# Kernel tuning notes

Measured on AMD Instinct MI355X. Metric: run time of the kernel, lower is better.

Reference implementation:

```python
import jax, jax.numpy as jnp
import numpy as np

DIM = 512
HID = 1024        # dim * expansion_factor
QK = 128          # query_key_dim
G = 256           # group_size
EPS = 1e-5


def setup_inputs() -> dict:
    key = jax.random.key(0)
    ks = jax.random.split(key, 6)
    x = jax.random.normal(ks[0], (4, 4096, DIM), jnp.float32)
    ln_w = jnp.ones((DIM,), jnp.float32)
    ln_b = jnp.zeros((DIM,), jnp.float32)
    Wh = 0.02 * jax.random.normal(ks[1], (DIM, 2 * HID), jnp.float32)
    bh = jnp.zeros((2 * HID,), jnp.float32)
    Wqk = 0.02 * jax.random.normal(ks[2], (DIM, QK), jnp.float32)
    bqk = jnp.zeros((QK,), jnp.float32)
    gamma = 0.02 * jax.random.normal(ks[3], (4, QK), jnp.float32)  # nn.init.normal_(gamma, std=0.02)
    beta = jnp.zeros((4, QK), jnp.float32)
    Wo = 0.02 * jax.random.normal(ks[4], (HID, DIM), jnp.float32)
    bo = jnp.zeros((DIM,), jnp.float32)
    return {"x": x, "ln_w": ln_w, "ln_b": ln_b, "Wh": Wh, "bh": bh,
            "Wqk": Wqk, "bqk": bqk, "gamma": gamma, "beta": beta,
            "Wo": Wo, "bo": bo}


def reference(x, ln_w, ln_b, Wh, bh, Wqk, bqk, gamma, beta, Wo, bo):
    b, n, _ = x.shape
    g = n // G  # number of groups (n chosen as multiple of G -> no padding)

    # LayerNorm (torch uses biased variance)
    mu = jnp.mean(x, axis=-1, keepdims=True)
    var = jnp.mean((x - mu) ** 2, axis=-1, keepdims=True)
    normed = (x - mu) * jax.lax.rsqrt(var + EPS) * ln_w + ln_b

    # to_hidden: Linear -> SiLU, split into v / gate
    h = jax.nn.silu(normed @ Wh + bh)            # [b, n, 2*HID]
    v, gate = jnp.split(h, 2, axis=-1)           # each [b, n, HID]

    # to_qk: Linear -> SiLU, then 4-head offset/scale
    qk = jax.nn.silu(normed @ Wqk + bqk)         # [b, n, QK]
    qkh = qk[..., None, :] * gamma + beta        # [b, n, 4, QK]
    quad_q, lin_q, quad_k, lin_k = (qkh[..., i, :] for i in range(4))

    # group: b (g n) d -> b g n d
    grp = lambda t: t.reshape(b, g, G, t.shape[-1])
    qq, qk_, lq, lk, vv = map(grp, (quad_q, quad_k, lin_q, lin_k, v))

    # quadratic (group-local) attention with ReLU^2 scores, causal within group
    sim = jnp.einsum('bgid,bgjd->bgij', qq, qk_) / G
    attn = jnp.square(jnp.maximum(sim, 0.0))
    causal_mask = jnp.triu(jnp.ones((G, G), dtype=bool), 1)
    attn = jnp.where(causal_mask, 0.0, attn)
    quad_out = jnp.einsum('bgij,bgje->bgie', attn, vv)   # [b, g, G, HID]

    # linear attention across groups: per-group kv, exclusive cumsum over group dim
    lin_kv = jnp.einsum('bgnd,bgne->bgde', lk, vv) / G   # [b, g, QK, HID]
    lin_kv = jnp.cumsum(lin_kv, axis=1)
    lin_kv = jnp.pad(lin_kv, ((0, 0), (1, 0), (0, 0), (0, 0)))[:, :-1]
    lin_out = jnp.einsum('bgde,bgnd->bgne', lin_kv, lq)  # [b, g, G, HID]

    out = gate * (quad_out.reshape(b, n, HID) + lin_out.reshape(b, n, HID))
    return out @ Wo + bo + x
```

## Files before the change

kernel.cpp:

```cpp
#include <hip/hip_runtime.h>
#include <hip/hip_bf16.h>
#include <math.h>


#define BATCH 4
#define SEQ   4096
#define TROWS 16384
#define DIMD  512
#define HIDD  1024
#define QKD   128
#define GRP   256
#define NGRP  16
#define BGRP  64
#define EPIW  132

typedef unsigned short bfraw;
typedef __attribute__((ext_vector_type(8))) short bf16x8;
typedef __attribute__((ext_vector_type(8))) unsigned short u16x8;
typedef __attribute__((ext_vector_type(4))) unsigned int u32x4;
typedef __attribute__((ext_vector_type(4))) float f32x4;

__device__ __forceinline__ float bf2f(bfraw u) {
    union { float f; unsigned int i; } c;
    c.i = ((unsigned int)u) << 16;
    return c.f;
}
__device__ __forceinline__ bfraw f2bf(float f) {
    unsigned int x = __float_as_uint(f);
    unsigned int r = (x + 0x7fffu + ((x >> 16) & 1u)) >> 16;
    return (bfraw)r;
}
__device__ __forceinline__ unsigned int pkbf(float lo, float hi) {
    __hip_bfloat162 h2 = __float22bfloat162_rn(make_float2(lo, hi));
    union { __hip_bfloat162 h; unsigned int u; } c; c.h = h2;
    return c.u;
}
__device__ __forceinline__ void store16bf(bfraw* dst, const float* src) {
    u32x4 a, b;
    #pragma unroll
    for (int k = 0; k < 4; ++k) a[k] = pkbf(src[2 * k], src[2 * k + 1]);
    #pragma unroll
    for (int k = 0; k < 4; ++k) b[k] = pkbf(src[8 + 2 * k], src[8 + 2 * k + 1]);
    *(u32x4*)dst = a;
    *(u32x4*)(dst + 8) = b;
}
__device__ __forceinline__ void store8bf(bfraw* dst, const float* src) {
    u32x4 a;
    #pragma unroll
    for (int k = 0; k < 4; ++k) a[k] = pkbf(src[2 * k], src[2 * k + 1]);
    *(u32x4*)dst = a;
}
__device__ __forceinline__ float silu_f(float z) {
    return z / (1.f + __expf(-z));
}
__device__ __forceinline__ void gload_lds16(const void* g, void* l) {
    __builtin_amdgcn_global_load_lds(
        (const __attribute__((address_space(1))) unsigned int*)g,
        (__attribute__((address_space(3))) unsigned int*)l, 16, 0, 0);
}

__device__ __forceinline__ void mfma_step(const bfraw* As, const bfraw* Bs,
                                          f32x4 acc[4][4], int wm, int wn,
                                          int q, int mi) {
    bf16x8 af[4], bfg[4];
    #pragma unroll
    for (int i = 0; i < 4; ++i)
        af[i] = *(const bf16x8*)&As[(size_t)(wm * 64 + i * 16 + mi) * 32 + q * 8];
    #pragma unroll
    for (int j = 0; j < 4; ++j)
        bfg[j] = *(const bf16x8*)&Bs[(size_t)(wn * 64 + j * 16 + mi) * 32 + q * 8];
    #pragma unroll
    for (int i = 0; i < 4; ++i)
        #pragma unroll
        for (int j = 0; j < 4; ++j)
            acc[i][j] = __builtin_amdgcn_mfma_f32_16x16x32_bf16(af[i], bfg[j], acc[i][j], 0, 0, 0);
}

#define SMEMP_DECL                                              \
    __shared__ __align__(16) char smem_[33280];                 \
    bfraw* A0buf = (bfraw*)smem_;                               \
    bfraw* B0buf = (bfraw*)(smem_ + 8192);                      \
    bfraw* A1buf = (bfraw*)(smem_ + 16384);                     \
    bfraw* B1buf = (bfraw*)(smem_ + 24576);

#define PIPE_DSTS                                               \
    bfraw* a0d  = A0buf + wid * 512;                            \
    bfraw* a0d2 = A0buf + 2048 + wid * 512;                     \
    bfraw* b0d  = B0buf + wid * 512;                            \
    bfraw* b0d2 = B0buf + 2048 + wid * 512;                     \
    bfraw* a1d  = A1buf + wid * 512;                            \
    bfraw* a1d2 = A1buf + 2048 + wid * 512;                     \
    bfraw* b1d  = B1buf + wid * 512;                            \
    bfraw* b1d2 = B1buf + 2048 + wid * 512;

#define KLOOP_PRE(Abase, Astr, Bbase, Bstr)                                    \
    const bfraw* pa0 = (Abase) + (size_t)(t >> 2) * (Astr) + (t & 3) * 8;      \
    const bfraw* pa1 = pa0 + (size_t)64 * (Astr);                              \
    const bfraw* pb0 = (Bbase) + (size_t)(t >> 2) * (Bstr) + (t & 3) * 8;      \
    const bfraw* pb1 = pb0 + (size_t)64 * (Bstr);

#define STAGE0                                                                 \
    do { gload_lds16(pa0, a0d); gload_lds16(pa1, a0d2);                        \
         gload_lds16(pb0, b0d); gload_lds16(pb1, b0d2);                        \
         pa0 += 32; pa1 += 32; pb0 += 32; pb1 += 32; } while (0)
#define STAGE1                                                                 \
    do { gload_lds16(pa0, a1d); gload_lds16(pa1, a1d2);                        \
         gload_lds16(pb0, b1d); gload_lds16(pb1, b1d2);                        \
         pa0 += 32; pa1 += 32; pb0 += 32; pb1 += 32; } while (0)

#define PIPE_LOOP(NIT, Abase, Astr, Bbase, Bstr)                               \
    {                                                                          \
        KLOOP_PRE(Abase, Astr, Bbase, Bstr)                                    \
        STAGE0;                                                                \
        for (int it = 0; it < (NIT); it += 2) {                                \
            __syncthreads();                                                   \
            if (it + 1 < (NIT)) STAGE1;                                        \
            mfma_step(A0buf, B0buf, acc, wm, wn, q, mi);                       \
            __syncthreads();                                                   \
            if (it + 2 < (NIT)) STAGE0;                                        \
            if (it + 1 < (NIT))                                                \
                mfma_step(A1buf, B1buf, acc, wm, wn, q, mi);                   \
        }                                                                      \
        __syncthreads();                                                       \
    }

__device__ __forceinline__ int epi_row(int p, int lr) {
    return (lr < 16) ? (p * 16 + lr) : (64 + p * 16 + (lr - 16));
}

__global__ __launch_bounds__(256) void prep_kernel(const float* __restrict__ x,
                                                   const float* __restrict__ lnw,
                                                   const float* __restrict__ lnb,
                                                   const float* __restrict__ Wh,
                                                   const float* __restrict__ Wo,
                                                   const float* __restrict__ Wqk,
                                                   bfraw* __restrict__ normb,
                                                   bfraw* __restrict__ WhT,
                                                   bfraw* __restrict__ WoT,
                                                   bfraw* __restrict__ WqkT) {
    __shared__ float tile[32][33];
    int bid = blockIdx.x;
    int t = threadIdx.x;
    if (bid < 4096) {
        int row  = bid * 4 + (t >> 6);
        int lane = t & 63;
        const float* xr = x + (size_t)row * DIMD;
        float4 v0 = ((const float4*)xr)[lane];
        float4 v1 = ((const float4*)xr)[lane + 64];
        float s  = v0.x + v0.y + v0.z + v0.w + v1.x + v1.y + v1.z + v1.w;
        float ss = v0.x*v0.x + v0.y*v0.y + v0.z*v0.z + v0.w*v0.w
                 + v1.x*v1.x + v1.y*v1.y + v1.z*v1.z + v1.w*v1.w;
        #pragma unroll
        for (int off = 32; off; off >>= 1) {
            s  += __shfl_xor(s, off);
            ss += __shfl_xor(ss, off);
        }
        float mu  = s * (1.f / DIMD);
        float var = ss * (1.f / DIMD) - mu * mu;
        float inv = rsqrtf(var + 1e-5f);
        float4 w0 = ((const float4*)lnw)[lane],  w1 = ((const float4*)lnw)[lane + 64];
        float4 b0 = ((const float4*)lnb)[lane],  b1 = ((const float4*)lnb)[lane + 64];
        unsigned int o0 = pkbf((v0.x - mu) * inv * w0.x + b0.x,
                               (v0.y - mu) * inv * w0.y + b0.y);
        unsigned int o1 = pkbf((v0.z - mu) * inv * w0.z + b0.z,
                               (v0.w - mu) * inv * w0.w + b0.w);
        unsigned int o2 = pkbf((v1.x - mu) * inv * w1.x + b1.x,
                               (v1.y - mu) * inv * w1.y + b1.y);
        unsigned int o3 = pkbf((v1.z - mu) * inv * w1.z + b1.z,
                               (v1.w - mu) * inv * w1.w + b1.w);
        unsigned int* brow = (unsigned int*)(normb + (size_t)row * DIMD);
        ((uint2*)brow)[lane]      = make_uint2(o0, o1);
        ((uint2*)brow)[lane + 64] = make_uint2(o2, o3);
        return;
    }
    bid -= 4096;
    const float* in; bfraw* outp; int R, C, nx;
    if (bid < 1024)      { in = Wh;  outp = WhT;  R = DIMD; C = 2 * HIDD; nx = 64; }
    else if (bid < 1536) { bid -= 1024; in = Wo;  outp = WoT;  R = HIDD; C = DIMD; nx = 16; }
    else                 { bid -= 1536; in = Wqk; outp = WqkT; R = DIMD; C = QKD;  nx = 4; }
    int c0 = (bid % nx) * 32, r0 = (bid / nx) * 32;
    int tr = t >> 3, tc4 = (t & 7) * 4;
    float4 v = *(const float4*)&in[(size_t)(r0 + tr) * C + c0 + tc4];
    tile[tr][tc4 + 0] = v.x; tile[tr][tc4 + 1] = v.y;
    tile[tr][tc4 + 2] = v.z; tile[tr][tc4 + 3] = v.w;
    __syncthreads();
    ushort4 s;
    s.x = f2bf(tile[tc4 + 0][tr]);
    s.y = f2bf(tile[tc4 + 1][tr]);
    s.z = f2bf(tile[tc4 + 2][tr]);
    s.w = f2bf(tile[tc4 + 3][tr]);
    *(ushort4*)&outp[(size_t)(c0 + tr) * R + r0 + tc4] = s;
}

__global__ __launch_bounds__(512, 4) void gemm_h256(
    const bfraw* __restrict__ A,
    const bfraw* __restrict__ WhT,
    const bfraw* __restrict__ WqkT,
    const float* __restrict__ bh,
    const float* __restrict__ bqk,
    const float* __restrict__ gamma,
    const float* __restrict__ beta,
    bfraw* __restrict__ vT,
    bfraw* __restrict__ gate,
    bfraw* __restrict__ qq,
    bfraw* __restrict__ lq,
    bfraw* __restrict__ kk,
    bfraw* __restrict__ lkT) {
    __shared__ __align__(16) char smem_[73728];
    const int t = threadIdx.x;
    const int lane = t & 63, wid = t >> 6;
    const int wm = wid >> 2, wn = wid & 3;
    const int q = lane >> 4, mi = lane & 15;
    int nid = (blockIdx.x & 7) * 144 + (blockIdx.x >> 3);
    const int ct = nid % 9, by = nid / 9;
    const int r0 = by * 128, c0 = ct * 256;
    const int bg = r0 >> 8;
    const int jb0 = r0 & 255;

    const int lslot = (t & 7) ^ ((t >> 3) & 7);
    const int srow  = 2 * (t >> 3) + (lslot >> 2);
    const int skel  = (lslot & 3) * 8;
    const bfraw* Asrc = A + (size_t)(r0 + srow) * DIMD + skel;
    const bfraw* Bsrc0;
    const bfraw* Bsrc1;
    if (ct < 8) {
        Bsrc0 = WhT + (size_t)(c0 + srow) * DIMD + skel;
        Bsrc1 = Bsrc0 + (size_t)128 * DIMD;
    } else {
        Bsrc0 = WqkT + (size_t)srow * DIMD + skel;
        Bsrc1 = Bsrc0;
    }
    const int swz = ((((mi & 1) << 2) | q) ^ ((mi >> 1) & 7)) << 4;
    const int a_off = (wm * 32 + (mi >> 1)) * 128 + swz;
    const int b_off = (wn * 32 + (mi >> 1)) * 128 + swz;

#define GH_STAGE(KT, SLOT)                                                    \
    do {                                                                      \
        char* sb_ = smem_ + (SLOT) * 24576;                                   \
        gload_lds16(Asrc  + (KT) * 32, sb_ + t * 16);                         \
        gload_lds16(Bsrc0 + (KT) * 32, sb_ + 8192 + t * 16);                  \
        gload_lds16(Bsrc1 + (KT) * 32, sb_ + 16384 + t * 16);                 \
    } while (0)

    f32x4 acc[4][4] = {};
    GH_STAGE(0, 0);
    GH_STAGE(1, 1);
    asm volatile("s_waitcnt vmcnt(3)" ::: "memory");
    __builtin_amdgcn_s_barrier();

    #pragma unroll
    for (int j = 0; j < 16; ++j) {
        if (j + 2 < 16) GH_STAGE(j + 2, (j + 2) % 3);
        const char* cb = smem_ + (j % 3) * 24576;
        bf16x8 af[4], bfr[4];
        #pragma unroll
        for (int mf = 0; mf < 4; ++mf)
            af[mf] = *(const bf16x8*)(cb + a_off + mf * 1024);
        #pragma unroll
        for (int nf = 0; nf < 4; ++nf)
            bfr[nf] = *(const bf16x8*)(cb + 8192 + b_off + nf * 1024);
        __builtin_amdgcn_s_setprio(1);
        #pragma unroll
        for (int mf = 0; mf < 4; ++mf)
            #pragma unroll
            for (int nf = 0; nf < 4; ++nf)
                acc[mf][nf] = __builtin_amdgcn_mfma_f32_16x16x32_bf16(
                    af[mf], bfr[nf], acc[mf][nf], 0, 0, 0);
        __builtin_amdgcn_s_setprio(0);
        if (j + 2 < 16)      asm volatile("s_waitcnt vmcnt(3)" ::: "memory");
        else if (j + 1 < 16) asm volatile("s_waitcnt vmcnt(0)" ::: "memory");
        __builtin_amdgcn_s_barrier();
    }
#undef GH_STAGE

    float* epi = (float*)smem_;
    if (ct == 8) {
        float* gbl = (float*)(smem_ + 36864);
        gbl[t] = gamma[t];
        gbl[t + 512] = beta[t];
        float bq4[4];
        #pragma unroll
        for (int nf = 0; nf < 4; ++nf)
            bq4[nf] = (wn < 2) ? bqk[wn * 64 + nf * 16 + mi] : 0.f;
        #pragma unroll
        for (int p2 = 0; p2 < 4; ++p2) {
            if (wm == (p2 >> 1) && wn < 2) {
                #pragma unroll
                for (int mf2 = 0; mf2 < 2; ++mf2) {
                    int mf = ((p2 & 1) << 1) + mf2;
                    #pragma unroll
                    for (int nf = 0; nf < 4; ++nf)
                        #pragma unroll
                        for (int rg = 0; rg < 4; ++rg)
                            epi[(mf2 * 16 + q * 4 + rg) * 132 + wn * 64 + nf * 16 + mi] =
                                silu_f(acc[mf][nf][rg] + bq4[nf]);
                }
            }
            __syncthreads();
            {
                int lr = t >> 4, cs = (t & 15) * 8;
                float z[8];
                #pragma unroll
                for (int k = 0; k < 8; ++k) z[k] = epi[lr * 132 + cs + k];
                size_t growr = (size_t)(r0 + p2 * 32 + lr) * QKD + cs;
                #pragma unroll
                for (int hd = 0; hd < 3; ++hd) {
                    bfraw* arr = (hd == 0) ? qq : (hd == 1) ? lq : kk;
                    float tmp[8];
                    #pragma unroll
                    for (int k = 0; k < 8; ++k)
                        tmp[k] = z[k] * gbl[hd * 128 + cs + k] + gbl[512 + hd * 128 + cs + k];
                    store8bf(arr + growr, tmp);
                }
            }
            {
                int c = t >> 2, jh = (t & 3) * 8;
                float g3 = gbl[384 + c], e3 = gbl[896 + c];
                float tmp[8];
                #pragma unroll
                for (int k = 0; k < 8; ++k)
                    tmp[k] = epi[(jh + k) * 132 + c] * g3 + e3;
                store8bf(lkT + ((size_t)bg * QKD + c) * GRP + jb0 + p2 * 32 + jh, tmp);
            }
            __syncthreads();
        }
        return;
    }
    float bias4[4];
    #pragma unroll
    for (int nf = 0; nf < 4; ++nf)
        bias4[nf] = bh[c0 + wn * 64 + nf * 16 + mi];
    if (ct < 4) {
        #pragma unroll
        for (int p2 = 0; p2 < 4; ++p2) {
            if (wm == (p2 >> 1)) {
                #pragma unroll
                for (int mf2 = 0; mf2 < 2; ++mf2) {
                    int mf = ((p2 & 1) << 1) + mf2;
                    #pragma unroll
                    for (int nf = 0; nf < 4; ++nf)
                        #pragma unroll
                        for (int rg = 0; rg < 4; ++rg)
                            epi[(mf2 * 16 + q * 4 + rg) * 257 + wn * 64 + nf * 16 + mi] =
                                silu_f(acc[mf][nf][rg] + bias4[nf]);
                }
            }
            __syncthreads();
            int e2 = t >> 1, js = (t & 1) * 16;
            float tmp[16];
            #pragma unroll
            for (int k = 0; k < 16; ++k)
                tmp[k] = epi[(js + k) * 257 + e2];
            store16bf(vT + ((size_t)bg * HIDD + c0 + e2) * GRP + jb0 + p2 * 32 + js, tmp);
            __syncthreads();
        }
    } else {
        #pragma unroll
        for (int p2 = 0; p2 < 4; ++p2) {
            if (wm == (p2 >> 1)) {
                #pragma unroll
                for (int mf2 = 0; mf2 < 2; ++mf2) {
                    int mf = ((p2 & 1) << 1) + mf2;
                    #pragma unroll
                    for (int nf = 0; nf < 4; ++nf)
                        #pragma unroll
                        for (int rg = 0; rg < 4; ++rg)
                            epi[(mf2 * 16 + q * 4 + rg) * 260 + wn * 64 + nf * 16 + mi] =
                                silu_f(acc[mf][nf][rg] + bias4[nf]);
                }
            }
            __syncthreads();
            int lr = t >> 4, cs = (t & 15) * 16;
            float tmp[16];
            #pragma unroll
            for (int k = 0; k < 16; ++k)
                tmp[k] = epi[lr * 260 + cs + k];
            store16bf(gate + (size_t)(r0 + p2 * 32 + lr) * HIDD + (c0 - HIDD) + cs, tmp);
            __syncthreads();
        }
    }
}

__global__ __launch_bounds__(256) void simkv_kernel(const bfraw* __restrict__ qq,
                                                    const bfraw* __restrict__ kk,
                                                    bfraw* __restrict__ attn,
                                                    const bfraw* __restrict__ vT,
                                                    const bfraw* __restrict__ lkT,
                                                    bfraw* __restrict__ kvT_raw) {
    SMEMP_DECL
    float* epi = (float*)smem_;
    int t = threadIdx.x;
    int lane = t & 63, wid = t >> 6;
    int wm = wid >> 1, wn = wid & 1;
    int q = lane >> 4, mi = lane & 15;
    int bid = blockIdx.x;
    f32x4 acc[4][4] = {};
    PIPE_DSTS
    if (bid < 512) {
        int bg = bid >> 3;
        int row0 = (bid & 7) * 128;
        PIPE_LOOP(8, vT + (size_t)bg * HIDD * GRP + (size_t)row0 * GRP, GRP,
                  lkT + (size_t)bg * QKD * GRP, GRP)
        bfraw* outg = kvT_raw + (size_t)bg * HIDD * QKD;
        #pragma unroll
        for (int p = 0; p < 4; ++p) {
            #pragma unroll
            for (int j = 0; j < 4; ++j)
                #pragma unroll
                for (int rg = 0; rg < 4; ++rg)
                    epi[(wm * 16 + q * 4 + rg) * EPIW + wn * 64 + j * 16 + mi] = acc[p][j][rg];
            __syncthreads();
            int lr = t >> 3, c0t = (t & 7) * 16;
            int gr = row0 + epi_row(p, lr);
            store16bf(outg + (size_t)gr * QKD + c0t, &epi[lr * EPIW + c0t]);
            __syncthreads();
        }
        return;
    }
    int i = bid - 512;
    int bg = i & 63;
    int tid = i >> 6;
    int ry = (tid == 0) ? 0 : 1;
    int rx = (tid == 2) ? 1 : 0;
    int row0 = ry * 128, col0 = rx * 128;
    PIPE_LOOP(4, qq + (size_t)(bg * GRP + row0) * QKD, QKD,
              kk + (size_t)(bg * GRP + col0) * QKD, QKD)
    bfraw* ag = attn + (size_t)bg * GRP * GRP;
    #pragma unroll
    for (int p = 0; p < 4; ++p) {
        #pragma unroll
        for (int j = 0; j < 4; ++j) {
            int colg = col0 + wn * 64 + j * 16 + mi;
            #pragma unroll
            for (int rg = 0; rg < 4; ++rg) {
                int rowg = row0 + wm * 64 + p * 16 + q * 4 + rg;
                float s = acc[p][j][rg] * (1.f / GRP);
                s = fmaxf(s, 0.f);
                s = s * s;
                epi[(wm * 16 + q * 4 + rg) * EPIW + wn * 64 + j * 16 + mi] =
                    (colg > rowg) ? 0.f : s;
            }
        }
        __syncthreads();
        int lr = t >> 3, c0t = (t & 7) * 16;
        int gr = row0 + epi_row(p, lr);
        store16bf(ag + (size_t)gr * GRP + col0 + c0t, &epi[lr * EPIW + c0t]);
        __syncthreads();
    }
}

__global__ __launch_bounds__(256) void cumsum2_kernel(const bfraw* __restrict__ raw,
                                                      bfraw* __restrict__ ex) {
    int idx = blockIdx.x * 256 + threadIdx.x;
    int b = idx >> 14;
    int r8 = (idx & 16383) * 8;
    const bfraw* rp = raw + (size_t)b * NGRP * 131072 + r8;
    bfraw* ep = ex + (size_t)b * NGRP * 131072 + r8;
    float run[8] = {};
    #pragma unroll
    for (int g = 0; g < NGRP; ++g) {
        u16x8 v = *(const u16x8*)(rp + (size_t)g * 131072);
        store8bf(ep + (size_t)g * 131072, run);
        #pragma unroll
        for (int k = 0; k < 8; ++k)
            run[k] += bf2f(v[k]) * (1.f / GRP);
    }
}

__global__ __launch_bounds__(512, 4) void quadlin256(
    const bfraw* __restrict__ attn,
    const bfraw* __restrict__ vT,
    const bfraw* __restrict__ lq,
    const bfraw* __restrict__ kvT_ex,
    const bfraw* __restrict__ gate,
    bfraw* __restrict__ gated) {
    __shared__ __align__(16) char smem_[73728];
    const int t = threadIdx.x;
    const int lane = t & 63, wid = t >> 6;
    const int wm = wid >> 2, wn = wid & 3;
    const int q = lane >> 4, mi = lane & 15;
    int nid = (blockIdx.x & 7) * 64 + (blockIdx.x >> 3);
    const int bg = nid >> 3;
    const int row0 = ((nid >> 2) & 1) * 128;
    const int c0 = (nid & 3) * 256;

    const int lslot = (t & 7) ^ ((t >> 3) & 7);
    const int srow  = 2 * (t >> 3) + (lslot >> 2);
    const int skel  = (lslot & 3) * 8;
    const bfraw* A1 = attn + ((size_t)bg * GRP + row0 + srow) * GRP + skel;
    const bfraw* B1a = vT + ((size_t)bg * HIDD + c0 + srow) * GRP + skel;
    const bfraw* B1b = B1a + (size_t)128 * GRP;
    const bfraw* A2 = lq + ((size_t)bg * GRP + row0 + srow) * QKD + skel;
    const bfraw* B2a = kvT_ex + ((size_t)bg * HIDD + c0 + srow) * QKD + skel;
    const bfraw* B2b = B2a + (size_t)128 * QKD;

    const int swz = ((((mi & 1) << 2) | q) ^ ((mi >> 1) & 7)) << 4;
    const int a_off = (wm * 32 + (mi >> 1)) * 128 + swz;
    const int b_off = (wn * 32 + (mi >> 1)) * 128 + swz;

#define QL_STAGE(PA, PB0, PB1, KT, SLOT)                                      \
    do {                                                                      \
        char* sb_ = smem_ + (SLOT) * 24576;                                   \
        gload_lds16((PA)  + (KT) * 32, sb_ + t * 16);                         \
        gload_lds16((PB0) + (KT) * 32, sb_ + 8192 + t * 16);                  \
        gload_lds16((PB1) + (KT) * 32, sb_ + 16384 + t * 16);                 \
    } while (0)
#define QL_MFMA(SLOT)                                                         \
    do {                                                                      \
        const char* cb = smem_ + (SLOT) * 24576;                              \
        bf16x8 af[4], bfr[4];                                                 \
        _Pragma("unroll")                                                     \
        for (int mf = 0; mf < 4; ++mf)                                        \
            af[mf] = *(const bf16x8*)(cb + a_off + mf * 1024);                \
        _Pragma("unroll")                                                     \
        for (int nf = 0; nf < 4; ++nf)                                        \
            bfr[nf] = *(const bf16x8*)(cb + 8192 + b_off + nf * 1024);        \
        __builtin_amdgcn_s_setprio(1);                                        \
        _Pragma("unroll")                                                     \
        for (int mf = 0; mf < 4; ++mf)                                        \
            _Pragma("unroll")                                                 \
            for (int nf = 0; nf < 4; ++nf)                                    \
                acc[mf][nf] = __builtin_amdgcn_mfma_f32_16x16x32_bf16(        \
                    af[mf], bfr[nf], acc[mf][nf], 0, 0, 0);                   \
        __builtin_amdgcn_s_setprio(0);                                        \
    } while (0)

    f32x4 acc[4][4] = {};
    const int nit1 = (row0 + 128) >> 5;
    QL_STAGE(A1, B1a, B1b, 0, 0);
    QL_STAGE(A1, B1a, B1b, 1, 1);
    asm volatile("s_waitcnt vmcnt(3)" ::: "memory");
    __builtin_amdgcn_s_barrier();
    for (int j = 0; j < nit1; ++j) {
        if (j + 2 < nit1) QL_STAGE(A1, B1a, B1b, j + 2, (j + 2) % 3);
        QL_MFMA(j % 3);
        if (j + 2 < nit1)      asm volatile("s_waitcnt vmcnt(3)" ::: "memory");
        else if (j + 1 < nit1) asm volatile("s_waitcnt vmcnt(0)" ::: "memory");
        __builtin_amdgcn_s_barrier();
    }
    QL_STAGE(A2, B2a, B2b, 0, 0);
    QL_STAGE(A2, B2a, B2b, 1, 1);
    asm volatile("s_waitcnt vmcnt(3)" ::: "memory");
    __builtin_amdgcn_s_barrier();
    #pragma unroll
    for (int j = 0; j < 4; ++j) {
        if (j + 2 < 4) QL_STAGE(A2, B2a, B2b, j + 2, (j + 2) % 3);
        QL_MFMA(j % 3);
        if (j + 2 < 4)      asm volatile("s_waitcnt vmcnt(3)" ::: "memory");
        else if (j + 1 < 4) asm volatile("s_waitcnt vmcnt(0)" ::: "memory");
        __builtin_amdgcn_s_barrier();
    }
#undef QL_STAGE
#undef QL_MFMA

    float* epi = (float*)smem_;
    #pragma unroll
    for (int p2 = 0; p2 < 4; ++p2) {
        if (wm == (p2 >> 1)) {
            #pragma unroll
            for (int mf2 = 0; mf2 < 2; ++mf2) {
                int mf = ((p2 & 1) << 1) + mf2;
                #pragma unroll
                for (int nf = 0; nf < 4; ++nf)
                    #pragma unroll
                    for (int rg = 0; rg < 4; ++rg)
                        epi[(mf2 * 16 + q * 4 + rg) * 260 + wn * 64 + nf * 16 + mi] =
                            acc[mf][nf][rg];
            }
        }
        __syncthreads();
        int lr = t >> 4, cs = (t & 15) * 16;
        size_t grow = (size_t)bg * GRP + row0 + p2 * 32 + lr;
        const float* src = epi + lr * 260 + cs;
        const bfraw* gsrc = gate + grow * HIDD + c0 + cs;
        u16x8 g0 = *(const u16x8*)gsrc;
        u16x8 g1 = *(const u16x8*)(gsrc + 8);
        float tmp[16];
        #pragma unroll
        for (int k = 0; k < 8; ++k) tmp[k] = src[k] * bf2f(g0[k]);
        #pragma unroll
        for (int k = 0; k < 8; ++k) tmp[8 + k] = src[8 + k] * bf2f(g1[k]);
        store16bf(gated + grow * HIDD + c0 + cs, tmp);
        __syncthreads();
    }
}

__global__ __launch_bounds__(1024, 4) void gemm_final(
    const bfraw* __restrict__ A,
    const bfraw* __restrict__ BT,
    const float* __restrict__ bo,
    const float* __restrict__ x,
    float* __restrict__ out) {
    __shared__ __align__(16) char smem_[147456];
    const int t = threadIdx.x;
    const int lane = t & 63, wid = t >> 6;
    const int wm = wid >> 2, wn = wid & 3;
    const int q = lane >> 4, mi = lane & 15;
    int nid = (blockIdx.x & 7) * 32 + (blockIdx.x >> 3);
    const int by = nid >> 2, cx = nid & 3;
    const int r0 = by * 256, c0 = cx * 128;

    const int lslot = (t & 7) ^ ((t >> 3) & 7);
    const int a_row = 2 * (t >> 3) + (lslot >> 2);
    const int a_kel = (lslot & 3) * 8;
    const bfraw* Asrc = A + (size_t)(r0 + a_row) * HIDD + a_kel;
    const int u = t & 511;
    const int lsb = (u & 7) ^ ((u >> 3) & 7);
    const int b_row = 2 * (u >> 3) + (lsb >> 2);
    const int b_kel = (lsb & 3) * 8 + (t >> 9) * 32;
    const bfraw* Bsrc = BT + (size_t)(c0 + b_row) * HIDD + b_kel;

    const int swz = ((((mi & 1) << 2) | q) ^ ((mi >> 1) & 7)) << 4;
    const int a_off = (wm * 32 + (mi >> 1)) * 128 + swz;
    const int b_off = (wn * 16 + (mi >> 1)) * 128 + swz;

#define GF_STAGE(SS, SLOT)                                                    \
    do {                                                                      \
        char* sb_ = smem_ + (SLOT) * 49152;                                   \
        gload_lds16(Asrc + (SS) * 64,      sb_ + t * 16);                     \
        gload_lds16(Asrc + (SS) * 64 + 32, sb_ + 16384 + t * 16);             \
        gload_lds16(Bsrc + (SS) * 64,      sb_ + 32768 + t * 16);             \
    } while (0)

    f32x4 acc[4][2] = {};
    GF_STAGE(0, 0);
    GF_STAGE(1, 1);
    asm volatile("s_waitcnt vmcnt(3)" ::: "memory");
    __builtin_amdgcn_s_barrier();

    #pragma unroll
    for (int ss = 0; ss < 16; ++ss) {
        if (ss + 2 < 16) GF_STAGE(ss + 2, (ss + 2) % 3);
        const char* cb = smem_ + (ss % 3) * 49152;
        #pragma unroll
        for (int h = 0; h < 2; ++h) {
            bf16x8 af[4], bfr[2];
            #pragma unroll
            for (int mf = 0; mf < 4; ++mf)
                af[mf] = *(const bf16x8*)(cb + h * 16384 + a_off + mf * 1024);
            #pragma unroll
            for (int nf = 0; nf < 2; ++nf)
                bfr[nf] = *(const bf16x8*)(cb + 32768 + h * 8192 + b_off + nf * 1024);
            __builtin_amdgcn_s_setprio(1);
            #pragma unroll
            for (int mf = 0; mf < 4; ++mf)
                #pragma unroll
                for (int nf = 0; nf < 2; ++nf)
                    acc[mf][nf] = __builtin_amdgcn_mfma_f32_16x16x32_bf16(
                        af[mf], bfr[nf], acc[mf][nf], 0, 0, 0);
            __builtin_amdgcn_s_setprio(0);
        }
        if (ss + 2 < 16)      asm volatile("s_waitcnt vmcnt(3)" ::: "memory");
        else if (ss + 1 < 16) asm volatile("s_waitcnt vmcnt(0)" ::: "memory");
        __builtin_amdgcn_s_barrier();
    }
#undef GF_STAGE

    float* epi = (float*)smem_;
    float bo2[2];
    #pragma unroll
    for (int nf = 0; nf < 2; ++nf)
        bo2[nf] = bo[c0 + wn * 32 + nf * 16 + mi];
    #pragma unroll
    for (int p = 0; p < 4; ++p) {
        if (wm == p) {
            #pragma unroll
            for (int mf = 0; mf < 4; ++mf)
                #pragma unroll
                for (int nf = 0; nf < 2; ++nf)
                    #pragma unroll
                    for (int rg = 0; rg < 4; ++rg)
                        epi[(mf * 16 + q * 4 + rg) * 132 + wn * 32 + nf * 16 + mi] =
                            acc[mf][nf][rg] + bo2[nf];
        }
        __syncthreads();
        int lr = t >> 4, cs = (t & 15) * 8;
        const float* src = epi + lr * 132 + cs;
        const float* xs = x + (size_t)(r0 + p * 64 + lr) * DIMD + c0 + cs;
        float* dst = out + (size_t)(r0 + p * 64 + lr) * DIMD + c0 + cs;
        #pragma unroll
        for (int v = 0; v < 2; ++v) {
            float4 a = ((const float4*)src)[v];
            float4 xv = ((const float4*)xs)[v];
            a.x += xv.x; a.y += xv.y; a.z += xv.z; a.w += xv.w;
            ((float4*)dst)[v] = a;
        }
        __syncthreads();
    }
}

extern "C" void kernel_launch(void* const* d_in, const int* in_sizes, int n_in,
                              void* d_out, int out_size, void* d_ws, size_t ws_size,
                              hipStream_t stream) {
    const float* x     = (const float*)d_in[0];
    const float* ln_w  = (const float*)d_in[1];
    const float* ln_b  = (const float*)d_in[2];
    const float* Wh    = (const float*)d_in[3];
    const float* bh    = (const float*)d_in[4];
    const float* Wqk   = (const float*)d_in[5];
    const float* bqk   = (const float*)d_in[6];
    const float* gamma = (const float*)d_in[7];
    const float* beta  = (const float*)d_in[8];
    const float* Wo    = (const float*)d_in[9];
    const float* bo    = (const float*)d_in[10];
    float* out = (float*)d_out;

    char* outb_ = (char*)d_out;
    bfraw* attn = (bfraw*)(outb_);
    bfraw* qq   = (bfraw*)(outb_ + 8388608);
    bfraw* kk   = (bfraw*)(outb_ + 12582912);
    bfraw* lq   = (bfraw*)(outb_ + 16777216);
    bfraw* WhT  = (bfraw*)(outb_ + 20971520);
    bfraw* WqkT = (bfraw*)(outb_ + 23068672);

    char* wsb = (char*)d_ws;
    bfraw* vT      = (bfraw*)(wsb);
    bfraw* gate    = (bfraw*)(wsb + 33554432);
    bfraw* gated   = (bfraw*)(wsb + 67108864);
    bfraw* normb   = (bfraw*)(wsb + 100663296);
    bfraw* kvT_raw = (bfraw*)(wsb + 117440512);
    bfraw* kvT_ex  = (bfraw*)(wsb + 134217728);
    bfraw* lkT     = (bfraw*)(wsb + 150994944);
    bfraw* WoT     = (bfraw*)(wsb + 155189248);

    prep_kernel<<<4096 + 1024 + 512 + 64, 256, 0, stream>>>(
        x, ln_w, ln_b, Wh, Wo, Wqk, normb, WhT, WoT, WqkT);
    gemm_h256<<<1152, 512, 0, stream>>>(
        normb, WhT, WqkT, bh, bqk, gamma, beta, vT, gate, qq, lq, kk, lkT);
    simkv_kernel<<<512 + 192, 256, 0, stream>>>(qq, kk, attn, vT, lkT, kvT_raw);
    cumsum2_kernel<<<(BATCH * QKD * HIDD) / 8 / 256, 256, 0, stream>>>(kvT_raw, kvT_ex);
    quadlin256<<<512, 512, 0, stream>>>(attn, vT, lq, kvT_ex, gate, gated);
    gemm_final<<<256, 1024, 0, stream>>>(gated, WoT, bo, x, out);
}
```

Before: 244.3 us.

## Enlarge hidden-projection GEMM tile to 256x256 with deeper K stages

The to_hidden/to_qk GEMM now uses 256-row by 256-column output tiles per block instead of 128x256, with K steps of 64 and double buffering (128 KB LDS) in place of K=32 triple buffering. Grid size halves to 576 blocks and each wave holds 8x4 MFMA accumulators. This raises arithmetic intensity and cuts redundant B-operand loads and barrier count. In exchange occupancy drops to one or two blocks per CU, register pressure rises, and fewer blocks may leave CUs underfilled.

Result: slower. 257.0 us (+5.2%).

```diff
diff --git a/kernel.cpp b/kernel.cpp
--- a/kernel.cpp
+++ b/kernel.cpp
@@ -192,7 +192,7 @@
     *(ushort4*)&outp[(size_t)(c0 + tr) * R + r0 + tc4] = s;
 }
 
-__global__ __launch_bounds__(512, 4) void gemm_h256(
+__global__ __launch_bounds__(512, 2) void gemm_h256(
     const bfraw* __restrict__ A,
     const bfraw* __restrict__ WhT,
     const bfraw* __restrict__ WqkT,
@@ -206,69 +206,76 @@
     bfraw* __restrict__ lq,
     bfraw* __restrict__ kk,
     bfraw* __restrict__ lkT) {
-    __shared__ __align__(16) char smem_[73728];
+    __shared__ __align__(16) char smem_[131072];
     const int t = threadIdx.x;
     const int lane = t & 63, wid = t >> 6;
     const int wm = wid >> 2, wn = wid & 3;
     const int q = lane >> 4, mi = lane & 15;
-    int nid = (blockIdx.x & 7) * 144 + (blockIdx.x >> 3);
+    int nid = (blockIdx.x & 7) * 72 + (blockIdx.x >> 3);
     const int ct = nid % 9, by = nid / 9;
-    const int r0 = by * 128, c0 = ct * 256;
-    const int bg = r0 >> 8;
-    const int jb0 = r0 & 255;
-
-    const int lslot = (t & 7) ^ ((t >> 3) & 7);
-    const int srow  = 2 * (t >> 3) + (lslot >> 2);
-    const int skel  = (lslot & 3) * 8;
-    const bfraw* Asrc = A + (size_t)(r0 + srow) * DIMD + skel;
-    const bfraw* Bsrc0;
-    const bfraw* Bsrc1;
+    const int r0 = by * 256, c0 = ct * 256;
+    const int bg = by;
+
+    const int rA = t >> 3;
+    const int sk = (((t & 7) ^ ((t >> 3) & 7))) * 8;
+    const bfraw* Asrc = A + (size_t)(r0 + rA) * DIMD + sk;
+    const bfraw* Bsrc;
+    const bfraw* Bsrc2;
     if (ct < 8) {
-        Bsrc0 = WhT + (size_t)(c0 + srow) * DIMD + skel;
-        Bsrc1 = Bsrc0 + (size_t)128 * DIMD;
+        Bsrc  = WhT + (size_t)(c0 + rA) * DIMD + sk;
+        Bsrc2 = Bsrc + (size_t)128 * DIMD;
     } else {
-        Bsrc0 = WqkT + (size_t)srow * DIMD + skel;
-        Bsrc1 = Bsrc0;
-    }
-    const int swz = ((((mi & 1) << 2) | q) ^ ((mi >> 1) & 7)) << 4;
-    const int a_off = (wm * 32 + (mi >> 1)) * 128 + swz;
-    const int b_off = (wn * 32 + (mi >> 1)) * 128 + swz;
-
-#define GH_STAGE(KT, SLOT)                                                    \
+        Bsrc  = WqkT + (size_t)rA * DIMD + sk;
+        Bsrc2 = Bsrc;
+    }
+    const int rsw = mi & 7;
+
+#define GH_STAGE(KT, BUF)                                                     \
     do {                                                                      \
-        char* sb_ = smem_ + (SLOT) * 24576;                                   \
-        gload_lds16(Asrc  + (KT) * 32, sb_ + t * 16);                         \
-        gload_lds16(Bsrc0 + (KT) * 32, sb_ + 8192 + t * 16);                  \
-        gload_lds16(Bsrc1 + (KT) * 32, sb_ + 16384 + t * 16);                 \
+        char* bb = smem_ + (BUF) * 65536;                                     \
+        const bfraw* a0 = Asrc + (KT) * 64;                                   \
+        const bfraw* b0 = Bsrc + (KT) * 64;                                   \
+        const bfraw* b2 = Bsrc2 + (KT) * 64;                                  \
+        gload_lds16(a0,                       bb + t * 16);                   \
+        gload_lds16(a0 + (size_t)64 * DIMD,   bb + 8192 + t * 16);            \
+        gload_lds16(a0 + (size_t)128 * DIMD,  bb + 16384 + t * 16);           \
+        gload_lds16(a0 + (size_t)192 * DIMD,  bb + 24576 + t * 16);           \
+        gload_lds16(b0,                       bb + 32768 + t * 16);           \
+        gload_lds16(b0 + (size_t)64 * DIMD,   bb + 40960 + t * 16);           \
+        gload_lds16(b2,                       bb + 49152 + t * 16);           \
+        gload_lds16(b2 + (size_t)64 * DIMD,   bb + 57344 + t * 16);           \
     } while (0)
 
-    f32x4 acc[4][4] = {};
+    f32x4 acc[8][4] = {};
     GH_STAGE(0, 0);
-    GH_STAGE(1, 1);
-    asm volatile("s_waitcnt vmcnt(3)" ::: "memory");
+    asm volatile("s_waitcnt vmcnt(0)" ::: "memory");
     __builtin_amdgcn_s_barrier();
 
     #pragma unroll
-    for (int j = 0; j < 16; ++j) {
-        if (j + 2 < 16) GH_STAGE(j + 2, (j + 2) % 3);
-        const char* cb = smem_ + (j % 3) * 24576;
-        bf16x8 af[4], bfr[4];
-        #pragma unroll
-        for (int mf = 0; mf < 4; ++mf)
-            af[mf] = *(const bf16x8*)(cb + a_off + mf * 1024);
-        #pragma unroll
-        for (int nf = 0; nf < 4; ++nf)
-            bfr[nf] = *(const bf16x8*)(cb + 8192 + b_off + nf * 1024);
-        __builtin_amdgcn_s_setprio(1);
-        #pragma unroll
-        for (int mf = 0; mf < 4; ++mf)
+    for (int kt = 0; kt < 8; ++kt) {
+        if (kt + 1 < 8) GH_STAGE(kt + 1, (kt + 1) & 1);
+        const char* cb = smem_ + (kt & 1) * 65536;
+        #pragma unroll
+        for (int ks = 0; ks < 2; ++ks) {
+            const int kb = ((ks * 4 + q) ^ rsw) << 4;
+            bf16x8 af[8], bfr[4];
+            #pragma unroll
+            for (int mf = 0; mf < 8; ++mf)
+                af[mf] = *(const bf16x8*)(cb + wm * 16384 + (mf * 16 + mi) * 128 + kb);
             #pragma unroll
             for (int nf = 0; nf < 4; ++nf)
-                acc[mf][nf] = __builtin_amdgcn_mfma_f32_16x16x32_bf16(
-                    af[mf], bfr[nf], acc[mf][nf], 0, 0, 0);
-        __builtin_amdgcn_s_setprio(0);
-        if (j + 2 < 16)      asm volatile("s_waitcnt vmcnt(3)" ::: "memory");
-        else if (j + 1 < 16) asm volatile("s_waitcnt vmcnt(0)" ::: "memory");
+                bfr[nf] = *(const bf16x8*)(cb + 32768 + (wn >> 1) * 16384 +
+                                           ((wn & 1) * 64 + nf * 16 + mi) * 128 + kb);
+            __builtin_amdgcn_s_setprio(1);
+            #pragma unroll
+            for (int mf = 0; mf < 8; ++mf)
+                #pragma unroll
+                for (int nf = 0; nf < 4; ++nf)
+                    acc[mf][nf] = __builtin_amdgcn_mfma_f32_16x16x32_bf16(
+                        af[mf], bfr[nf], acc[mf][nf], 0, 0, 0);
+            __builtin_amdgcn_s_setprio(0);
+        }
+        if (kt + 1 < 8) asm volatile("s_waitcnt vmcnt(0)" ::: "memory");
         __builtin_amdgcn_s_barrier();
     }
 #undef GH_STAGE
@@ -283,11 +290,11 @@
         for (int nf = 0; nf < 4; ++nf)
             bq4[nf] = (wn < 2) ? bqk[wn * 64 + nf * 16 + mi] : 0.f;
         #pragma unroll
-        for (int p2 = 0; p2 < 4; ++p2) {
-            if (wm == (p2 >> 1) && wn < 2) {
+        for (int p = 0; p < 8; ++p) {
+            if (wm == (p >> 2) && wn < 2) {
                 #pragma unroll
                 for (int mf2 = 0; mf2 < 2; ++mf2) {
-                    int mf = ((p2 & 1) << 1) + mf2;
+                    int mf = ((p & 3) << 1) + mf2;
                     #pragma unroll
                     for (int nf = 0; nf < 4; ++nf)
                         #pragma unroll
@@ -302,7 +309,7 @@
                 float z[8];
                 #pragma unroll
                 for (int k = 0; k < 8; ++k) z[k] = epi[lr * 132 + cs + k];
-                size_t growr = (size_t)(r0 + p2 * 32 + lr) * QKD + cs;
+                size_t growr = (size_t)(r0 + p * 32 + lr) * QKD + cs;
                 #pragma unroll
                 for (int hd = 0; hd < 3; ++hd) {
                     bfraw* arr = (hd == 0) ? qq : (hd == 1) ? lq : kk;
@@ -320,7 +327,7 @@
                 #pragma unroll
                 for (int k = 0; k < 8; ++k)
                     tmp[k] = epi[(jh + k) * 132 + c] * g3 + e3;
-                store8bf(lkT + ((size_t)bg * QKD + c) * GRP + jb0 + p2 * 32 + jh, tmp);
+                store8bf(lkT + ((size_t)bg * QKD + c) * GRP + p * 32 + jh, tmp);
             }
             __syncthreads();
         }
@@ -332,11 +339,11 @@
         bias4[nf] = bh[c0 + wn * 64 + nf * 16 + mi];
     if (ct < 4) {
         #pragma unroll
-        for (int p2 = 0; p2 < 4; ++p2) {
-            if (wm == (p2 >> 1)) {
+        for (int p = 0; p < 8; ++p) {
+            if (wm == (p >> 2)) {
                 #pragma unroll
                 for (int mf2 = 0; mf2 < 2; ++mf2) {
-                    int mf = ((p2 & 1) << 1) + mf2;
+                    int mf = ((p & 3) << 1) + mf2;
                     #pragma unroll
                     for (int nf = 0; nf < 4; ++nf)
                         #pragma unroll
@@ -351,16 +358,16 @@
             #pragma unroll
             for (int k = 0; k < 16; ++k)
                 tmp[k] = epi[(js + k) * 257 + e2];
-            store16bf(vT + ((size_t)bg * HIDD + c0 + e2) * GRP + jb0 + p2 * 32 + js, tmp);
+            store16bf(vT + ((size_t)bg * HIDD + c0 + e2) * GRP + p * 32 + js, tmp);
             __syncthreads();
         }
     } else {
         #pragma unroll
-        for (int p2 = 0; p2 < 4; ++p2) {
-            if (wm == (p2 >> 1)) {
+        for (int p = 0; p < 8; ++p) {
+            if (wm == (p >> 2)) {
                 #pragma unroll
                 for (int mf2 = 0; mf2 < 2; ++mf2) {
-                    int mf = ((p2 & 1) << 1) + mf2;
+                    int mf = ((p & 3) << 1) + mf2;
                     #pragma unroll
                     for (int nf = 0; nf < 4; ++nf)
                         #pragma unroll
@@ -375,7 +382,7 @@
             #pragma unroll
             for (int k = 0; k < 16; ++k)
                 tmp[k] = epi[lr * 260 + cs + k];
-            store16bf(gate + (size_t)(r0 + p2 * 32 + lr) * HIDD + (c0 - HIDD) + cs, tmp);
+            store16bf(gate + (size_t)(r0 + p * 32 + lr) * HIDD + (c0 - HIDD) + cs, tmp);
             __syncthreads();
         }
     }
@@ -725,7 +732,7 @@
 
     prep_kernel<<<4096 + 1024 + 512 + 64, 256, 0, stream>>>(
         x, ln_w, ln_b, Wh, Wo, Wqk, normb, WhT, WoT, WqkT);
-    gemm_h256<<<1152, 512, 0, stream>>>(
+    gemm_h256<<<576, 512, 0, stream>>>(
         normb, WhT, WqkT, bh, bqk, gamma, beta, vT, gate, qq, lq, kk, lkT);
     simkv_kernel<<<512 + 192, 256, 0, stream>>>(qq, kk, attn, vT, lkT, kvT_raw);
     cumsum2_kernel<<<(BATCH * QKD * HIDD) / 8 / 256, 256, 0, stream>>>(kvT_raw, kvT_ex);
```
